# Optimization experiments

Measured on AMD Instinct MI355X. Metric: run time of the kernel, lower is better.

## Reference

```python
import jax, jax.numpy as jnp
import numpy as np
from jax import lax

KERNEL_SIZES = (3, 5, 7)
EPS = 1e-12  # torch F.normalize default eps


def _gamma(x, k):
    """SpatialCorrelationSampler(kernel_size=k)(x, F.normalize(x, dim=1)).

    With patch_size=1, stride=1, padding=0, dilation=1 the sampler output at
    (b, y, x) is sum over channels and the kxk window of in1 * in2. Since
    in2 = in1 / max(||in1||_c, eps), the channel contraction collapses to
    ||x||^2 / max(||x||, eps) per pixel, followed by a kxk box-sum (VALID).
    x: [B, C, H, W] -> gamma: [B, H-k+1, W-k+1]
    """
    norm = jnp.sqrt(jnp.sum(x * x, axis=1))          # [B, H, W]
    p = (norm * norm) / jnp.maximum(norm, EPS)       # [B, H, W]
    return lax.reduce_window(p, 0.0, lax.add, (1, k, k), (1, 1, 1), 'VALID')


def reference(out_feat0, out_feat1, gt_feat0, gt_feat1):
    loss = jnp.float32(0.0)
    for xo, xg in ((out_feat0, gt_feat0), (out_feat1, gt_feat1)):
        for k in KERNEL_SIZES:
            go = _gamma(xo, k)
            gg = _gamma(xg, k)
            loss = loss + jnp.mean((go - gg) ** 2)   # nn.MSELoss (mean)
    return loss


def setup_inputs() -> dict:
    key = jax.random.key(0)
    k0, k1, k2, k3 = jax.random.split(key, 4)
    return {
        'out_feat0': jax.random.normal(k0, (8, 256, 64, 64), dtype=jnp.float32),
        'out_feat1': jax.random.normal(k1, (8, 512, 32, 32), dtype=jnp.float32),
        'gt_feat0': jax.random.normal(k2, (8, 256, 64, 64), dtype=jnp.float32),
        'gt_feat1': jax.random.normal(k3, (8, 512, 32, 32), dtype=jnp.float32),
    }
```

## Files before the change

kernel.cpp:

```cpp
#include <hip/hip_runtime.h>
#include <math.h>

#define EPS 1e-12f

typedef float f4 __attribute__((ext_vector_type(4)));

template <int PLANE, int C, int CS_N>
__device__ __forceinline__ void partial_tile(
    const float* __restrict__ xo, const float* __restrict__ xg,
    float* __restrict__ part,
    int b, int tile, int cs, int tid, float* lds )
{
    constexpr int SLABF = 256;
    constexpr int CG    = 8;
    constexpr int CPT   = (C / CS_N) / CG;
    static_assert(CPT == 8, "geometry");

    const int quad = tid & 63;
    const int cg   = tid >> 6;
    const int base = b * C * PLANE + tile * SLABF + quad * 4;
    const int c0   = cs * (C / CS_N) + cg * CPT;

    f4 so = {0.f, 0.f, 0.f, 0.f};
    f4 sg = {0.f, 0.f, 0.f, 0.f};
#pragma unroll
    for (int ib = 0; ib < CPT / 4; ++ib) {
        f4 vo[4], vg[4];
#pragma unroll
        for (int u = 0; u < 4; ++u) {
            const int off = base + (c0 + ib * 4 + u) * PLANE;
            vo[u] = *reinterpret_cast<const f4*>(xo + off);
            vg[u] = *reinterpret_cast<const f4*>(xg + off);
        }
#pragma unroll
        for (int u = 0; u < 4; ++u) {
            so += vo[u] * vo[u];
            sg += vg[u] * vg[u];
        }
    }

    *reinterpret_cast<f4*>(lds + (0 * CG + cg) * SLABF + quad * 4) = so;
    *reinterpret_cast<f4*>(lds + (1 * CG + cg) * SLABF + quad * 4) = sg;
    __syncthreads();

    if (tid < 128) {
        const int s = tid >> 6;
        const int q = tid & 63;
        f4 a = {0.f, 0.f, 0.f, 0.f};
#pragma unroll
        for (int g = 0; g < CG; ++g)
            a += *reinterpret_cast<const f4*>(lds + (s * CG + g) * SLABF + q * 4);
        *reinterpret_cast<f4*>(
            part + ((s * 8 + b) * CS_N + cs) * PLANE + tile * SLABF + q * 4) = a;
    }
}

__global__ __launch_bounds__(512) void stage1a_kernel(
    const float* __restrict__ o0, const float* __restrict__ g0,
    const float* __restrict__ o1, const float* __restrict__ g1,
    float* __restrict__ part0, float* __restrict__ part1,
    float* __restrict__ out)
{
    __shared__ float lds[4096];
    const int bid = blockIdx.x;
    if (bid == 0 && threadIdx.x == 0) out[0] = 0.0f;
    if (bid < 512) {
        const int b = bid >> 6, tile = (bid >> 2) & 15, cs = bid & 3;
        partial_tile<4096, 256, 4>(o0, g0, part0, b, tile, cs, threadIdx.x, lds);
    } else {
        const int e = bid - 512;
        const int b = e >> 5, tile = (e >> 3) & 3, cs = e & 7;
        partial_tile<1024, 512, 8>(o1, g1, part1, b, tile, cs, threadIdx.x, lds);
    }
}

template <int H, int K, int CS>
__device__ __forceinline__ void tile_mse(
    const float* __restrict__ po, const float* __restrict__ pg,
    float* __restrict__ out, int tid,
    float* d , float* rbuf , float* wsum )
{
    constexpr int V = H - K + 1;
    constexpr int PLANE = H * H;

    for (int q = tid; q < PLANE / 4; q += 512) {
        f4 ao = {0.f, 0.f, 0.f, 0.f};
        f4 ag = {0.f, 0.f, 0.f, 0.f};
#pragma unroll
        for (int c = 0; c < CS; ++c) {
            ao += *reinterpret_cast<const f4*>(po + c * PLANE + q * 4);
            ag += *reinterpret_cast<const f4*>(pg + c * PLANE + q * 4);
        }
        f4 dd;
#pragma unroll
        for (int j = 0; j < 4; ++j) {
            const float no = sqrtf(ao[j]);
            const float ng = sqrtf(ag[j]);
            dd[j] = ao[j] / fmaxf(no, EPS) - ag[j] / fmaxf(ng, EPS);
        }
        *reinterpret_cast<f4*>(d + q * 4) = dd;
    }
    __syncthreads();

    for (int i = tid; i < H * V; i += 512) {
        const int y = i / V;
        const int x = i - y * V;
        float s = 0.f;
#pragma unroll
        for (int j = 0; j < K; ++j) s += d[y * H + x + j];
        rbuf[i] = s;
    }
    __syncthreads();

    float acc = 0.f;
    for (int i = tid; i < V * V; i += 512) {
        const int y = i / V;
        const int x = i - y * V;
        float s = 0.f;
#pragma unroll
        for (int j = 0; j < K; ++j) s += rbuf[(y + j) * V + x];
        acc = fmaf(s, s, acc);
    }

    for (int off = 32; off > 0; off >>= 1) acc += __shfl_down(acc, off);
    if ((tid & 63) == 0) wsum[tid >> 6] = acc;
    __syncthreads();
    if (tid == 0) {
        float total = 0.f;
#pragma unroll
        for (int wv = 0; wv < 8; ++wv) total += wsum[wv];
        atomicAdd(out, total / (float)(8 * V * V));
    }
}

__global__ __launch_bounds__(512) void stage2_kernel(
    const float* __restrict__ part0, const float* __restrict__ part1,
    float* __restrict__ out)
{
    __shared__ float d[4096];
    __shared__ float rbuf[64 * 62];
    __shared__ float wsum[8];

    const int bid = blockIdx.x;
    const int t   = bid / 24;
    const int rem = bid % 24;
    const int b   = rem / 3;
    const int ki  = rem % 3;
    const int tid = threadIdx.x;

    if (t == 0) {
        const float* po = part0 + (0 * 8 + b) * 4 * 4096;
        const float* pg = part0 + (1 * 8 + b) * 4 * 4096;
        if      (ki == 0) tile_mse<64, 3, 4>(po, pg, out, tid, d, rbuf, wsum);
        else if (ki == 1) tile_mse<64, 5, 4>(po, pg, out, tid, d, rbuf, wsum);
        else              tile_mse<64, 7, 4>(po, pg, out, tid, d, rbuf, wsum);
    } else {
        const float* po = part1 + (0 * 8 + b) * 8 * 1024;
        const float* pg = part1 + (1 * 8 + b) * 8 * 1024;
        if      (ki == 0) tile_mse<32, 3, 8>(po, pg, out, tid, d, rbuf, wsum);
        else if (ki == 1) tile_mse<32, 5, 8>(po, pg, out, tid, d, rbuf, wsum);
        else              tile_mse<32, 7, 8>(po, pg, out, tid, d, rbuf, wsum);
    }
}

extern "C" void kernel_launch(void* const* d_in, const int* in_sizes, int n_in,
                              void* d_out, int out_size, void* d_ws, size_t ws_size,
                              hipStream_t stream) {
    const float* out_feat0 = (const float*)d_in[0];
    const float* out_feat1 = (const float*)d_in[1];
    const float* gt_feat0  = (const float*)d_in[2];
    const float* gt_feat1  = (const float*)d_in[3];
    float* out = (float*)d_out;

    float* part0 = (float*)d_ws;
    float* part1 = part0 + 2 * 8 * 4 * 4096;

    stage1a_kernel<<<768, 512, 0, stream>>>(
        out_feat0, gt_feat0, out_feat1, gt_feat1, part0, part1, out);
    stage2_kernel<<<48, 512, 0, stream>>>(part0, part1, out);
}
```

Before: 122.4 us.

## Fuse two stages into one kernel with per-batch atomic ticket handoff

Merges the channel-reduction stage and the box-sum/MSE stage into a single launch. Each block takes an atomic ticket per (tensor, batch) group; the last three blocks of a group spin until the group is complete and then compute the three kernel-size MSE terms. A final ticket counter makes the last finisher sum the 48 partial results deterministically. This removes the second kernel launch and the gap between kernels, at the cost of an added memset, spin-waiting blocks and more LDS per block.

```diff
diff --git a/kernel.cpp b/kernel.cpp
--- a/kernel.cpp
+++ b/kernel.cpp
@@ -55,30 +55,10 @@
     }
 }
 
-__global__ __launch_bounds__(512) void stage1a_kernel(
-    const float* __restrict__ o0, const float* __restrict__ g0,
-    const float* __restrict__ o1, const float* __restrict__ g1,
-    float* __restrict__ part0, float* __restrict__ part1,
-    float* __restrict__ out)
-{
-    __shared__ float lds[4096];
-    const int bid = blockIdx.x;
-    if (bid == 0 && threadIdx.x == 0) out[0] = 0.0f;
-    if (bid < 512) {
-        const int b = bid >> 6, tile = (bid >> 2) & 15, cs = bid & 3;
-        partial_tile<4096, 256, 4>(o0, g0, part0, b, tile, cs, threadIdx.x, lds);
-    } else {
-        const int e = bid - 512;
-        const int b = e >> 5, tile = (e >> 3) & 3, cs = e & 7;
-        partial_tile<1024, 512, 8>(o1, g1, part1, b, tile, cs, threadIdx.x, lds);
-    }
-}
-
 template <int H, int K, int CS>
-__device__ __forceinline__ void tile_mse(
-    const float* __restrict__ po, const float* __restrict__ pg,
-    float* __restrict__ out, int tid,
-    float* d , float* rbuf , float* wsum )
+__device__ __forceinline__ float tile_mse(
+    const float* __restrict__ po, const float* __restrict__ pg, int tid,
+    float* d , float* rbuf, float* wsum)
 {
     constexpr int V = H - K + 1;
     constexpr int PLANE = H * H;
@@ -125,41 +105,89 @@
     for (int off = 32; off > 0; off >>= 1) acc += __shfl_down(acc, off);
     if ((tid & 63) == 0) wsum[tid >> 6] = acc;
     __syncthreads();
+    float total = 0.f;
     if (tid == 0) {
-        float total = 0.f;
 #pragma unroll
         for (int wv = 0; wv < 8; ++wv) total += wsum[wv];
-        atomicAdd(out, total / (float)(8 * V * V));
-    }
-}
-
-__global__ __launch_bounds__(512) void stage2_kernel(
-    const float* __restrict__ part0, const float* __restrict__ part1,
+        total /= (float)(8 * V * V);
+    }
+    return total;
+}
+
+__global__ __launch_bounds__(512) void fused_kernel(
+    const float* __restrict__ o0, const float* __restrict__ g0,
+    const float* __restrict__ o1, const float* __restrict__ g1,
+    float* __restrict__ part0, float* __restrict__ part1,
+    unsigned* __restrict__ ctrl,
+    float* __restrict__ msebuf,
     float* __restrict__ out)
 {
-    __shared__ float d[4096];
+    __shared__ float lds[4096];
     __shared__ float rbuf[64 * 62];
     __shared__ float wsum[8];
+    __shared__ unsigned s_tk;
 
     const int bid = blockIdx.x;
-    const int t   = bid / 24;
-    const int rem = bid % 24;
-    const int b   = rem / 3;
-    const int ki  = rem % 3;
     const int tid = threadIdx.x;
 
+    int t, b, g, N;
+    if (bid < 512) {
+        t = 0; b = bid >> 6;
+        const int tile = (bid >> 2) & 15, cs = bid & 3;
+        partial_tile<4096, 256, 4>(o0, g0, part0, b, tile, cs, tid, lds);
+        g = b; N = 64;
+    } else {
+        t = 1;
+        const int e = bid - 512; b = e >> 5;
+        const int tile = (e >> 3) & 3, cs = e & 7;
+        partial_tile<1024, 512, 8>(o1, g1, part1, b, tile, cs, tid, lds);
+        g = 8 + b; N = 32;
+    }
+
+    __syncthreads();
+
+    if (tid == 0)
+        s_tk = __hip_atomic_fetch_add(&ctrl[g], 1u,
+                                      __ATOMIC_ACQ_REL, __HIP_MEMORY_SCOPE_AGENT);
+    __syncthreads();
+    const int tk = (int)s_tk;
+    if (tk < N - 3) return;
+    const int ki = N - 1 - tk;
+
+    if (tid == 0) {
+        while (__hip_atomic_load(&ctrl[g], __ATOMIC_ACQUIRE,
+                                 __HIP_MEMORY_SCOPE_AGENT) != (unsigned)N) {
+            __builtin_amdgcn_s_sleep(1);
+        }
+    }
+    __syncthreads();
+
+    float s = 0.f;
     if (t == 0) {
         const float* po = part0 + (0 * 8 + b) * 4 * 4096;
         const float* pg = part0 + (1 * 8 + b) * 4 * 4096;
-        if      (ki == 0) tile_mse<64, 3, 4>(po, pg, out, tid, d, rbuf, wsum);
-        else if (ki == 1) tile_mse<64, 5, 4>(po, pg, out, tid, d, rbuf, wsum);
-        else              tile_mse<64, 7, 4>(po, pg, out, tid, d, rbuf, wsum);
+        if      (ki == 0) s = tile_mse<64, 3, 4>(po, pg, tid, lds, rbuf, wsum);
+        else if (ki == 1) s = tile_mse<64, 5, 4>(po, pg, tid, lds, rbuf, wsum);
+        else              s = tile_mse<64, 7, 4>(po, pg, tid, lds, rbuf, wsum);
     } else {
         const float* po = part1 + (0 * 8 + b) * 8 * 1024;
         const float* pg = part1 + (1 * 8 + b) * 8 * 1024;
-        if      (ki == 0) tile_mse<32, 3, 8>(po, pg, out, tid, d, rbuf, wsum);
-        else if (ki == 1) tile_mse<32, 5, 8>(po, pg, out, tid, d, rbuf, wsum);
-        else              tile_mse<32, 7, 8>(po, pg, out, tid, d, rbuf, wsum);
+        if      (ki == 0) s = tile_mse<32, 3, 8>(po, pg, tid, lds, rbuf, wsum);
+        else if (ki == 1) s = tile_mse<32, 5, 8>(po, pg, tid, lds, rbuf, wsum);
+        else              s = tile_mse<32, 7, 8>(po, pg, tid, lds, rbuf, wsum);
+    }
+
+    if (tid == 0) {
+        msebuf[g * 3 + ki] = s;
+        const unsigned t2 = __hip_atomic_fetch_add(
+            &ctrl[16], 1u, __ATOMIC_ACQ_REL, __HIP_MEMORY_SCOPE_AGENT);
+        if (t2 == 47u) {
+            float tot = 0.f;
+            for (int i = 0; i < 48; ++i)
+                tot += __hip_atomic_load(&msebuf[i], __ATOMIC_RELAXED,
+                                         __HIP_MEMORY_SCOPE_AGENT);
+            out[0] = tot;
+        }
     }
 }
 
@@ -172,10 +200,13 @@
     const float* gt_feat1  = (const float*)d_in[3];
     float* out = (float*)d_out;
 
-    float* part0 = (float*)d_ws;
-    float* part1 = part0 + 2 * 8 * 4 * 4096;
-
-    stage1a_kernel<<<768, 512, 0, stream>>>(
-        out_feat0, gt_feat0, out_feat1, gt_feat1, part0, part1, out);
-    stage2_kernel<<<48, 512, 0, stream>>>(part0, part1, out);
-}
+    float*    part0  = (float*)d_ws;
+    float*    part1  = part0 + 2 * 8 * 4 * 4096;
+    unsigned* ctrl   = (unsigned*)((char*)d_ws + (2u << 20));
+    float*    msebuf = (float*)((char*)d_ws + (2u << 20) + 256);
+
+    hipMemsetAsync(ctrl, 0, 128, stream);
+    fused_kernel<<<768, 512, 0, stream>>>(
+        out_feat0, gt_feat0, out_feat1, gt_feat1,
+        part0, part1, ctrl, msebuf, out);
+}
```

Result: slower. 165.0 us (+34.8%).

## Repartition stage-1 channel reduction into more channel splits with smaller blocks

Applied to the files above, without the earlier changes.

Stage 1 now uses 256-thread blocks, each covering 16 channels over a 1024-pixel tile, instead of 512-thread blocks covering 64 or 64 channels over 256 pixels. The channel splits grow from 4/8 to 16/32, so each thread keeps four f4 accumulators across a non-unrolled 4-channel loop, and the LDS reduction runs in four synchronised rounds. The aim is to change per-block memory access patterns and occupancy. In exchange, the partial buffer is four times larger, so stage 2 (only 48 blocks) must read 16–32 partial planes per pixel, which adds traffic to a lightly parallel stage.

```diff
diff --git a/kernel.cpp b/kernel.cpp
--- a/kernel.cpp
+++ b/kernel.cpp
@@ -11,66 +11,65 @@
     float* __restrict__ part,
     int b, int tile, int cs, int tid, float* lds )
 {
-    constexpr int SLABF = 256;
-    constexpr int CG    = 8;
-    constexpr int CPT   = (C / CS_N) / CG;
-    static_assert(CPT == 8, "geometry");
+    const int lane = tid & 63;
+    const int cg   = tid >> 6;
+    const int c0   = cs * 16 + cg * 4;
+    const int base = b * C * PLANE + tile * 1024 + lane * 4;
 
-    const int quad = tid & 63;
-    const int cg   = tid >> 6;
-    const int base = b * C * PLANE + tile * SLABF + quad * 4;
-    const int c0   = cs * (C / CS_N) + cg * CPT;
-
-    f4 so = {0.f, 0.f, 0.f, 0.f};
-    f4 sg = {0.f, 0.f, 0.f, 0.f};
-#pragma unroll
-    for (int ib = 0; ib < CPT / 4; ++ib) {
+    f4 ao[4] = {{0,0,0,0},{0,0,0,0},{0,0,0,0},{0,0,0,0}};
+    f4 ag[4] = {{0,0,0,0},{0,0,0,0},{0,0,0,0},{0,0,0,0}};
+#pragma unroll 1
+    for (int ch = 0; ch < 4; ++ch) {
+        const int coff = base + (c0 + ch) * PLANE;
         f4 vo[4], vg[4];
 #pragma unroll
-        for (int u = 0; u < 4; ++u) {
-            const int off = base + (c0 + ib * 4 + u) * PLANE;
-            vo[u] = *reinterpret_cast<const f4*>(xo + off);
-            vg[u] = *reinterpret_cast<const f4*>(xg + off);
-        }
+        for (int j = 0; j < 4; ++j)
+            vo[j] = *reinterpret_cast<const f4*>(xo + coff + j * 256);
 #pragma unroll
-        for (int u = 0; u < 4; ++u) {
-            so += vo[u] * vo[u];
-            sg += vg[u] * vg[u];
+        for (int j = 0; j < 4; ++j)
+            vg[j] = *reinterpret_cast<const f4*>(xg + coff + j * 256);
+#pragma unroll
+        for (int j = 0; j < 4; ++j) {
+            ao[j] += vo[j] * vo[j];
+            ag[j] += vg[j] * vg[j];
         }
     }
 
-    *reinterpret_cast<f4*>(lds + (0 * CG + cg) * SLABF + quad * 4) = so;
-    *reinterpret_cast<f4*>(lds + (1 * CG + cg) * SLABF + quad * 4) = sg;
-    __syncthreads();
-
-    if (tid < 128) {
-        const int s = tid >> 6;
-        const int q = tid & 63;
-        f4 a = {0.f, 0.f, 0.f, 0.f};
 #pragma unroll
-        for (int g = 0; g < CG; ++g)
-            a += *reinterpret_cast<const f4*>(lds + (s * CG + g) * SLABF + q * 4);
-        *reinterpret_cast<f4*>(
-            part + ((s * 8 + b) * CS_N + cs) * PLANE + tile * SLABF + q * 4) = a;
+    for (int j = 0; j < 4; ++j) {
+        *reinterpret_cast<f4*>(lds + (0 * 4 + cg) * 256 + lane * 4) = ao[j];
+        *reinterpret_cast<f4*>(lds + (1 * 4 + cg) * 256 + lane * 4) = ag[j];
+        __syncthreads();
+        if (tid < 128) {
+            const int s = tid >> 6;
+            const int q = tid & 63;
+            f4 a = {0.f, 0.f, 0.f, 0.f};
+#pragma unroll
+            for (int g = 0; g < 4; ++g)
+                a += *reinterpret_cast<const f4*>(lds + (s * 4 + g) * 256 + q * 4);
+            *reinterpret_cast<f4*>(
+                part + ((s * 8 + b) * CS_N + cs) * PLANE + tile * 1024 + j * 256 + q * 4) = a;
+        }
+        __syncthreads();
     }
 }
 
-__global__ __launch_bounds__(512) void stage1a_kernel(
+__global__ __launch_bounds__(256) void stage1_kernel(
     const float* __restrict__ o0, const float* __restrict__ g0,
     const float* __restrict__ o1, const float* __restrict__ g1,
     float* __restrict__ part0, float* __restrict__ part1,
     float* __restrict__ out)
 {
-    __shared__ float lds[4096];
+    __shared__ float lds[2048];
     const int bid = blockIdx.x;
     if (bid == 0 && threadIdx.x == 0) out[0] = 0.0f;
     if (bid < 512) {
-        const int b = bid >> 6, tile = (bid >> 2) & 15, cs = bid & 3;
-        partial_tile<4096, 256, 4>(o0, g0, part0, b, tile, cs, threadIdx.x, lds);
+        const int b = bid >> 6, tile = (bid >> 4) & 3, cs = bid & 15;
+        partial_tile<4096, 256, 16>(o0, g0, part0, b, tile, cs, threadIdx.x, lds);
     } else {
         const int e = bid - 512;
-        const int b = e >> 5, tile = (e >> 3) & 3, cs = e & 7;
-        partial_tile<1024, 512, 8>(o1, g1, part1, b, tile, cs, threadIdx.x, lds);
+        const int b = e >> 5, cs = e & 31;
+        partial_tile<1024, 512, 32>(o1, g1, part1, b, 0, cs, threadIdx.x, lds);
     }
 }
 
@@ -86,7 +85,7 @@
     for (int q = tid; q < PLANE / 4; q += 512) {
         f4 ao = {0.f, 0.f, 0.f, 0.f};
         f4 ag = {0.f, 0.f, 0.f, 0.f};
-#pragma unroll
+#pragma unroll 4
         for (int c = 0; c < CS; ++c) {
             ao += *reinterpret_cast<const f4*>(po + c * PLANE + q * 4);
             ag += *reinterpret_cast<const f4*>(pg + c * PLANE + q * 4);
@@ -149,17 +148,17 @@
     const int tid = threadIdx.x;
 
     if (t == 0) {
-        const float* po = part0 + (0 * 8 + b) * 4 * 4096;
-        const float* pg = part0 + (1 * 8 + b) * 4 * 4096;
-        if      (ki == 0) tile_mse<64, 3, 4>(po, pg, out, tid, d, rbuf, wsum);
-        else if (ki == 1) tile_mse<64, 5, 4>(po, pg, out, tid, d, rbuf, wsum);
-        else              tile_mse<64, 7, 4>(po, pg, out, tid, d, rbuf, wsum);
+        const float* po = part0 + (0 * 8 + b) * 16 * 4096;
+        const float* pg = part0 + (1 * 8 + b) * 16 * 4096;
+        if      (ki == 0) tile_mse<64, 3, 16>(po, pg, out, tid, d, rbuf, wsum);
+        else if (ki == 1) tile_mse<64, 5, 16>(po, pg, out, tid, d, rbuf, wsum);
+        else              tile_mse<64, 7, 16>(po, pg, out, tid, d, rbuf, wsum);
     } else {
-        const float* po = part1 + (0 * 8 + b) * 8 * 1024;
-        const float* pg = part1 + (1 * 8 + b) * 8 * 1024;
-        if      (ki == 0) tile_mse<32, 3, 8>(po, pg, out, tid, d, rbuf, wsum);
-        else if (ki == 1) tile_mse<32, 5, 8>(po, pg, out, tid, d, rbuf, wsum);
-        else              tile_mse<32, 7, 8>(po, pg, out, tid, d, rbuf, wsum);
+        const float* po = part1 + (0 * 8 + b) * 32 * 1024;
+        const float* pg = part1 + (1 * 8 + b) * 32 * 1024;
+        if      (ki == 0) tile_mse<32, 3, 32>(po, pg, out, tid, d, rbuf, wsum);
+        else if (ki == 1) tile_mse<32, 5, 32>(po, pg, out, tid, d, rbuf, wsum);
+        else              tile_mse<32, 7, 32>(po, pg, out, tid, d, rbuf, wsum);
     }
 }
 
@@ -173,9 +172,9 @@
     float* out = (float*)d_out;
 
     float* part0 = (float*)d_ws;
-    float* part1 = part0 + 2 * 8 * 4 * 4096;
+    float* part1 = part0 + 2 * 8 * 16 * 4096;
 
-    stage1a_kernel<<<768, 512, 0, stream>>>(
+    stage1_kernel<<<768, 256, 0, stream>>>(
         out_feat0, gt_feat0, out_feat1, gt_feat1, part0, part1, out);
     stage2_kernel<<<48, 512, 0, stream>>>(part0, part1, out);
 }
```

Result: slower. 130.5 us (+6.6%).

## Split channel reduction into per-8-channel partial planes, drop LDS reduce in stage1

Applied to the files above, without the earlier changes.

Stage 1 now has each block compute sums of squares over 8-channel groups for whole planes of one tensor, writing many more partial planes (32 or 64 per batch) instead of reducing across channel groups in LDS. This removes the LDS staging and barrier from stage 1. In exchange, stage 2 must read and sum far more partial data (8x more) in only 48 blocks, which adds workspace traffic and latency to the serial tail.

```diff
diff --git a/kernel.cpp b/kernel.cpp
--- a/kernel.cpp
+++ b/kernel.cpp
@@ -6,71 +6,48 @@
 typedef float f4 __attribute__((ext_vector_type(4)));
 
 template <int PLANE, int C, int CS_N>
-__device__ __forceinline__ void partial_tile(
-    const float* __restrict__ xo, const float* __restrict__ xg,
+__device__ __forceinline__ void sq_partial(
+    const float* __restrict__ src,
     float* __restrict__ part,
-    int b, int tile, int cs, int tid, float* lds )
+    int sslot, int b, int ch0, int tid)
 {
-    constexpr int SLABF = 256;
-    constexpr int CG    = 8;
-    constexpr int CPT   = (C / CS_N) / CG;
-    static_assert(CPT == 8, "geometry");
+    constexpr int QP = PLANE / 4;
+    const float* sb = src + b * C * PLANE;
 
-    const int quad = tid & 63;
-    const int cg   = tid >> 6;
-    const int base = b * C * PLANE + tile * SLABF + quad * 4;
-    const int c0   = cs * (C / CS_N) + cg * CPT;
-
-    f4 so = {0.f, 0.f, 0.f, 0.f};
-    f4 sg = {0.f, 0.f, 0.f, 0.f};
 #pragma unroll
-    for (int ib = 0; ib < CPT / 4; ++ib) {
-        f4 vo[4], vg[4];
+    for (int r = 0; r < 2; ++r) {
+        const int tau = tid + r * 512;
+        const int sub = tau / QP;
+        const int q   = tau - sub * QP;
+        const int c0  = ch0 + sub * 8;
+        f4 acc = {0.f, 0.f, 0.f, 0.f};
 #pragma unroll
-        for (int u = 0; u < 4; ++u) {
-            const int off = base + (c0 + ib * 4 + u) * PLANE;
-            vo[u] = *reinterpret_cast<const f4*>(xo + off);
-            vg[u] = *reinterpret_cast<const f4*>(xg + off);
+        for (int c = 0; c < 8; ++c) {
+            const f4 v = *reinterpret_cast<const f4*>(sb + (c0 + c) * PLANE + q * 4);
+            acc += v * v;
         }
-#pragma unroll
-        for (int u = 0; u < 4; ++u) {
-            so += vo[u] * vo[u];
-            sg += vg[u] * vg[u];
-        }
-    }
-
-    *reinterpret_cast<f4*>(lds + (0 * CG + cg) * SLABF + quad * 4) = so;
-    *reinterpret_cast<f4*>(lds + (1 * CG + cg) * SLABF + quad * 4) = sg;
-    __syncthreads();
-
-    if (tid < 128) {
-        const int s = tid >> 6;
-        const int q = tid & 63;
-        f4 a = {0.f, 0.f, 0.f, 0.f};
-#pragma unroll
-        for (int g = 0; g < CG; ++g)
-            a += *reinterpret_cast<const f4*>(lds + (s * CG + g) * SLABF + q * 4);
         *reinterpret_cast<f4*>(
-            part + ((s * 8 + b) * CS_N + cs) * PLANE + tile * SLABF + q * 4) = a;
+            part + ((sslot * 8 + b) * CS_N + (ch0 >> 3) + sub) * PLANE + q * 4) = acc;
     }
 }
 
-__global__ __launch_bounds__(512) void stage1a_kernel(
+__global__ __launch_bounds__(512) void stage1_kernel(
     const float* __restrict__ o0, const float* __restrict__ g0,
     const float* __restrict__ o1, const float* __restrict__ g1,
     float* __restrict__ part0, float* __restrict__ part1,
     float* __restrict__ out)
 {
-    __shared__ float lds[4096];
     const int bid = blockIdx.x;
-    if (bid == 0 && threadIdx.x == 0) out[0] = 0.0f;
+    const int tid = threadIdx.x;
+    if (bid == 0 && tid == 0) out[0] = 0.0f;
+
     if (bid < 512) {
-        const int b = bid >> 6, tile = (bid >> 2) & 15, cs = bid & 3;
-        partial_tile<4096, 256, 4>(o0, g0, part0, b, tile, cs, threadIdx.x, lds);
+        const int s = bid >> 8, b = (bid >> 5) & 7, cs = bid & 31;
+        sq_partial<4096, 256, 32>(s ? g0 : o0, part0, s, b, cs * 8, tid);
     } else {
         const int e = bid - 512;
-        const int b = e >> 5, tile = (e >> 3) & 3, cs = e & 7;
-        partial_tile<1024, 512, 8>(o1, g1, part1, b, tile, cs, threadIdx.x, lds);
+        const int s = e >> 7, b = (e >> 4) & 7, g = e & 15;
+        sq_partial<1024, 512, 64>(s ? g1 : o1, part1, s, b, g * 32, tid);
     }
 }
 
@@ -86,7 +63,7 @@
     for (int q = tid; q < PLANE / 4; q += 512) {
         f4 ao = {0.f, 0.f, 0.f, 0.f};
         f4 ag = {0.f, 0.f, 0.f, 0.f};
-#pragma unroll
+#pragma unroll 8
         for (int c = 0; c < CS; ++c) {
             ao += *reinterpret_cast<const f4*>(po + c * PLANE + q * 4);
             ag += *reinterpret_cast<const f4*>(pg + c * PLANE + q * 4);
@@ -149,17 +126,17 @@
     const int tid = threadIdx.x;
 
     if (t == 0) {
-        const float* po = part0 + (0 * 8 + b) * 4 * 4096;
-        const float* pg = part0 + (1 * 8 + b) * 4 * 4096;
-        if      (ki == 0) tile_mse<64, 3, 4>(po, pg, out, tid, d, rbuf, wsum);
-        else if (ki == 1) tile_mse<64, 5, 4>(po, pg, out, tid, d, rbuf, wsum);
-        else              tile_mse<64, 7, 4>(po, pg, out, tid, d, rbuf, wsum);
+        const float* po = part0 + (0 * 8 + b) * 32 * 4096;
+        const float* pg = part0 + (1 * 8 + b) * 32 * 4096;
+        if      (ki == 0) tile_mse<64, 3, 32>(po, pg, out, tid, d, rbuf, wsum);
+        else if (ki == 1) tile_mse<64, 5, 32>(po, pg, out, tid, d, rbuf, wsum);
+        else              tile_mse<64, 7, 32>(po, pg, out, tid, d, rbuf, wsum);
     } else {
-        const float* po = part1 + (0 * 8 + b) * 8 * 1024;
-        const float* pg = part1 + (1 * 8 + b) * 8 * 1024;
-        if      (ki == 0) tile_mse<32, 3, 8>(po, pg, out, tid, d, rbuf, wsum);
-        else if (ki == 1) tile_mse<32, 5, 8>(po, pg, out, tid, d, rbuf, wsum);
-        else              tile_mse<32, 7, 8>(po, pg, out, tid, d, rbuf, wsum);
+        const float* po = part1 + (0 * 8 + b) * 64 * 1024;
+        const float* pg = part1 + (1 * 8 + b) * 64 * 1024;
+        if      (ki == 0) tile_mse<32, 3, 64>(po, pg, out, tid, d, rbuf, wsum);
+        else if (ki == 1) tile_mse<32, 5, 64>(po, pg, out, tid, d, rbuf, wsum);
+        else              tile_mse<32, 7, 64>(po, pg, out, tid, d, rbuf, wsum);
     }
 }
 
@@ -173,9 +150,9 @@
     float* out = (float*)d_out;
 
     float* part0 = (float*)d_ws;
-    float* part1 = part0 + 2 * 8 * 4 * 4096;
+    float* part1 = part0 + 2 * 8 * 32 * 4096;
 
-    stage1a_kernel<<<768, 512, 0, stream>>>(
+    stage1_kernel<<<768, 512, 0, stream>>>(
         out_feat0, gt_feat0, out_feat1, gt_feat1, part0, part1, out);
     stage2_kernel<<<48, 512, 0, stream>>>(part0, part1, out);
 }
```

Measured after the change: 135.3 us. 1.11x slower.
